# Performance work log

Measured on AMD Instinct MI355X. Metric: run time of the kernel, lower is better.

## Reference

```python
import jax, jax.numpy as jnp
import numpy as np

K = 12  # kNN neighbors (includes self, as in PyG knn(x, x, k))
EPS = 1e-5


def bn(h, g, b):
    # Training-mode BatchNorm over all axes except the last (feature) axis.
    ax = tuple(range(h.ndim - 1))
    m = h.mean(axis=ax, keepdims=True)
    v = h.var(axis=ax, keepdims=True)  # biased variance, as BN uses
    return g * (h - m) * jax.lax.rsqrt(v + EPS) + b


def edge_conv(x, W1, b1, g, be, W2, b2):
    # x: [B, N, C] -> [B, N, H]. Dynamic kNN graph in feature space per graph.
    d2 = jnp.sum(x * x, axis=-1)                                  # [B, N]
    dist = d2[:, :, None] + d2[:, None, :] - 2.0 * jnp.einsum('bic,bjc->bij', x, x)
    _, idx = jax.lax.top_k(-dist, K)                              # [B, N, K]
    xj = jnp.take_along_axis(x[:, None, :, :], idx[:, :, :, None], axis=2)  # [B,N,K,C]
    xi = jnp.broadcast_to(x[:, :, None, :], xj.shape)
    e = jnp.concatenate([xi, xj - xi], axis=-1)                   # [B,N,K,2C]
    h = jax.nn.relu(bn(jnp.einsum('bnkc,ch->bnkh', e, W1) + b1, g, be))
    h = jnp.einsum('bnkh,ho->bnko', h, W2) + b2
    return h.mean(axis=2)                                         # mean aggr over K


def setup_inputs() -> dict:
    key = jax.random.key(0)
    ks = jax.random.split(key, 8)
    B, N, C, H, Hf, O = 32, 1024, 3, 64, 32, 2
    s = 0.1
    return {
        'x': jax.random.normal(ks[0], (B, N, C), jnp.float32),
        'w0a': jax.random.normal(ks[1], (2 * C, H), jnp.float32) * s,
        'b0a': jnp.zeros((H,), jnp.float32),
        'g0': jnp.ones((H,), jnp.float32),
        'be0': jnp.zeros((H,), jnp.float32),
        'w0b': jax.random.normal(ks[2], (H, H), jnp.float32) * s,
        'b0b': jnp.zeros((H,), jnp.float32),
        'wa': jax.random.normal(ks[3], (3, 2 * H, H), jnp.float32) * s,
        'ba': jnp.zeros((3, H), jnp.float32),
        'ga': jnp.ones((3, H), jnp.float32),
        'bea': jnp.zeros((3, H), jnp.float32),
        'wb': jax.random.normal(ks[4], (3, H, H), jnp.float32) * s,
        'bb': jnp.zeros((3, H), jnp.float32),
        'wf1': jax.random.normal(ks[5], (H, Hf), jnp.float32) * s,
        'bf1': jnp.zeros((Hf,), jnp.float32),
        'gf': jnp.ones((Hf,), jnp.float32),
        'bef': jnp.zeros((Hf,), jnp.float32),
        'wf2': jax.random.normal(ks[6], (Hf, O), jnp.float32) * s,
        'bf2': jnp.zeros((O,), jnp.float32),
    }


def reference(x, w0a, b0a, g0, be0, w0b, b0b, wa, ba, ga, bea, wb, bb,
              wf1, bf1, gf, bef, wf2, bf2):
    # Layer 0: input channels = 3
    h = edge_conv(x, w0a, b0a, g0, be0, w0b, b0b)
    # Layers 1..3: input channels = hidden
    for i in range(3):
        h = edge_conv(h, wa[i], ba[i], ga[i], bea[i], wb[i], bb[i])
    pooled = h.mean(axis=1)  # global_mean_pool over nodes -> [B, H]
    z = jax.nn.relu(bn(pooled @ wf1 + bf1, gf, bef))
    return z @ wf2 + bf2     # [B, 2]
```

## Files before the change

kernel.cpp:

```cpp
#include <hip/hip_runtime.h>
#include <cstddef>

#define BATCH 32
#define NPTS  1024
#define K_NN  12
#define HID   64
#define BN_EPS 1e-5f

typedef short bf16x8 __attribute__((ext_vector_type(8)));
typedef float f32x4 __attribute__((ext_vector_type(4)));

__device__ __forceinline__ unsigned long long dkey(float dval, int j) {
  int di = __float_as_int(dval);
  unsigned m = (unsigned)(di >> 31) | 0x80000000u;
  unsigned u = (unsigned)di ^ m;
  return ((unsigned long long)u << 32) | (unsigned)j;
}

__device__ __forceinline__ void cas_u64(unsigned long long &a, unsigned long long &b) {
  unsigned long long x = a, y = b;
  bool c = y < x;
  a = c ? y : x;
  b = c ? x : y;
}

__device__ __forceinline__ void sort16_u64(unsigned long long (&k)[16]) {
  cas_u64(k[0],k[1]);  cas_u64(k[2],k[3]);  cas_u64(k[4],k[5]);  cas_u64(k[6],k[7]);
  cas_u64(k[8],k[9]);  cas_u64(k[10],k[11]); cas_u64(k[12],k[13]); cas_u64(k[14],k[15]);
  cas_u64(k[0],k[2]);  cas_u64(k[1],k[3]);  cas_u64(k[4],k[6]);  cas_u64(k[5],k[7]);
  cas_u64(k[8],k[10]); cas_u64(k[9],k[11]); cas_u64(k[12],k[14]); cas_u64(k[13],k[15]);
  cas_u64(k[1],k[2]);  cas_u64(k[5],k[6]);  cas_u64(k[9],k[10]); cas_u64(k[13],k[14]);
  cas_u64(k[0],k[4]);  cas_u64(k[1],k[5]);  cas_u64(k[2],k[6]);  cas_u64(k[3],k[7]);
  cas_u64(k[8],k[12]); cas_u64(k[9],k[13]); cas_u64(k[10],k[14]); cas_u64(k[11],k[15]);
  cas_u64(k[2],k[4]);  cas_u64(k[3],k[5]);  cas_u64(k[10],k[12]); cas_u64(k[11],k[13]);
  cas_u64(k[1],k[2]);  cas_u64(k[3],k[4]);  cas_u64(k[5],k[6]);
  cas_u64(k[9],k[10]); cas_u64(k[11],k[12]); cas_u64(k[13],k[14]);
  cas_u64(k[0],k[8]);  cas_u64(k[1],k[9]);  cas_u64(k[2],k[10]); cas_u64(k[3],k[11]);
  cas_u64(k[4],k[12]); cas_u64(k[5],k[13]); cas_u64(k[6],k[14]); cas_u64(k[7],k[15]);
  cas_u64(k[4],k[8]);  cas_u64(k[5],k[9]);  cas_u64(k[6],k[10]); cas_u64(k[7],k[11]);
  cas_u64(k[2],k[4]);  cas_u64(k[3],k[5]);  cas_u64(k[6],k[8]);  cas_u64(k[7],k[9]);
  cas_u64(k[10],k[12]); cas_u64(k[11],k[13]);
  cas_u64(k[1],k[2]);  cas_u64(k[3],k[4]);  cas_u64(k[5],k[6]);  cas_u64(k[7],k[8]);
  cas_u64(k[9],k[10]); cas_u64(k[11],k[12]); cas_u64(k[13],k[14]);
}

__device__ __forceinline__ void merge12_u64(unsigned long long (&L)[12],
                                            const unsigned long long* S) {
#pragma unroll
  for (int i = 0; i < 12; ++i) {
    unsigned long long s = S[11 - i];
    L[i] = L[i] < s ? L[i] : s;
  }
  cas_u64(L[0],L[8]);  cas_u64(L[1],L[9]);  cas_u64(L[2],L[10]); cas_u64(L[3],L[11]);
  cas_u64(L[4],L[8]);  cas_u64(L[5],L[9]);  cas_u64(L[6],L[10]); cas_u64(L[7],L[11]);
  cas_u64(L[0],L[2]);  cas_u64(L[1],L[3]);  cas_u64(L[4],L[6]);  cas_u64(L[5],L[7]);
  cas_u64(L[8],L[10]); cas_u64(L[9],L[11]);
  cas_u64(L[0],L[1]);  cas_u64(L[2],L[3]);  cas_u64(L[4],L[5]);  cas_u64(L[6],L[7]);
  cas_u64(L[8],L[9]);  cas_u64(L[10],L[11]);
}

__global__ __launch_bounds__(512, 2) void knn64_mfma_kernel(
    const unsigned short* __restrict__ xh, const unsigned short* __restrict__ xm,
    const unsigned short* __restrict__ xl, const float* __restrict__ d2,
    int* __restrict__ idx,
    const float* __restrict__ hxi, const float* __restrict__ hxj,
    float* __restrict__ partial) {
  const int b    = blockIdx.y;
  const int lane = threadIdx.x & 63;
  const int wv_u = __builtin_amdgcn_readfirstlane(threadIdx.x >> 6);
  const int i0   = blockIdx.x * 64;
  const size_t bbase = (size_t)b * NPTS;
  const float* d2b = d2 + bbase;

  constexpr int NE = 8 * K_NN;
  __shared__ __align__(16) char smem[60416];
  unsigned short* alds = (unsigned short*)smem;
  float* slab = (float*)(smem + 25600 + wv_u * 4352);
  unsigned long long* lk = (unsigned long long*)smem;
  int* jlds = (int*)(smem + 49664);
  float* red1 = (float*)smem;
  float* red2 = (float*)(smem + 2048);

  const int qr = lane >> 4;
  const int lr = lane & 15;

  for (int it = threadIdx.x; it < 1536; it += 512) {
    const int row = it / 24, rem = it % 24, pl = rem >> 3, seg = rem & 7;
    const unsigned short* src = (pl == 0) ? xh : ((pl == 1) ? xm : xl);
    *(bf16x8*)(alds + row * 200 + pl * 64 + seg * 8) =
        *(const bf16x8*)(src + (bbase + i0 + row) * HID + seg * 8);
  }
  __syncthreads();

  unsigned long long L[K_NN];
#pragma unroll
  for (int k = 0; k < K_NN; ++k) L[k] = ~0ULL;

  const int j0 = wv_u * 128;

  bf16x8 Bh0, Bh1, Bm0, Bm1, Bl0, Bl1;
  {
    const size_t brow = (bbase + j0 + lr) * HID;
    Bh0 = *(const bf16x8*)(xh + brow + 0  + qr * 8);
    Bh1 = *(const bf16x8*)(xh + brow + 32 + qr * 8);
    Bm0 = *(const bf16x8*)(xm + brow + 0  + qr * 8);
    Bm1 = *(const bf16x8*)(xm + brow + 32 + qr * 8);
    Bl0 = *(const bf16x8*)(xl + brow + 0  + qr * 8);
    Bl1 = *(const bf16x8*)(xl + brow + 32 + qr * 8);
  }

#pragma unroll 1
  for (int chunk = 0; chunk < 8; ++chunk) {
    const int jb = j0 + chunk * 16;
    const bf16x8 bh0 = Bh0, bh1 = Bh1, bm0 = Bm0, bm1 = Bm1, bl0 = Bl0, bl1 = Bl1;

    f32x4 acc[4];
#pragma unroll
    for (int isub = 0; isub < 4; ++isub) acc[isub] = f32x4{0.f, 0.f, 0.f, 0.f};

#pragma unroll
    for (int isub = 0; isub < 4; ++isub) {
      const int ar = (isub * 16 + lr) * 200;
      bf16x8 Ah0 = *(const bf16x8*)(alds + ar + 0   + qr * 8);
      bf16x8 Ah1 = *(const bf16x8*)(alds + ar + 32  + qr * 8);
      bf16x8 Am0 = *(const bf16x8*)(alds + ar + 64  + qr * 8);
      bf16x8 Am1 = *(const bf16x8*)(alds + ar + 96  + qr * 8);
      bf16x8 Al0 = *(const bf16x8*)(alds + ar + 128 + qr * 8);
      bf16x8 Al1 = *(const bf16x8*)(alds + ar + 160 + qr * 8);
      f32x4 a = acc[isub];
      a = __builtin_amdgcn_mfma_f32_16x16x32_bf16(Ah0, bh0, a, 0, 0, 0);
      a = __builtin_amdgcn_mfma_f32_16x16x32_bf16(Ah1, bh1, a, 0, 0, 0);
      a = __builtin_amdgcn_mfma_f32_16x16x32_bf16(Ah0, bm0, a, 0, 0, 0);
      a = __builtin_amdgcn_mfma_f32_16x16x32_bf16(Ah1, bm1, a, 0, 0, 0);
      a = __builtin_amdgcn_mfma_f32_16x16x32_bf16(Am0, bh0, a, 0, 0, 0);
      a = __builtin_amdgcn_mfma_f32_16x16x32_bf16(Am1, bh1, a, 0, 0, 0);
      a = __builtin_amdgcn_mfma_f32_16x16x32_bf16(Ah0, bl0, a, 0, 0, 0);
      a = __builtin_amdgcn_mfma_f32_16x16x32_bf16(Ah1, bl1, a, 0, 0, 0);
      a = __builtin_amdgcn_mfma_f32_16x16x32_bf16(Al0, bh0, a, 0, 0, 0);
      a = __builtin_amdgcn_mfma_f32_16x16x32_bf16(Al1, bh1, a, 0, 0, 0);
      a = __builtin_amdgcn_mfma_f32_16x16x32_bf16(Am0, bm0, a, 0, 0, 0);
      a = __builtin_amdgcn_mfma_f32_16x16x32_bf16(Am1, bm1, a, 0, 0, 0);
      acc[isub] = a;
    }

    if (chunk < 7) {
      const size_t nrow = (bbase + jb + 16 + lr) * HID;
      Bh0 = *(const bf16x8*)(xh + nrow + 0  + qr * 8);
      Bh1 = *(const bf16x8*)(xh + nrow + 32 + qr * 8);
      Bm0 = *(const bf16x8*)(xm + nrow + 0  + qr * 8);
      Bm1 = *(const bf16x8*)(xm + nrow + 32 + qr * 8);
      Bl0 = *(const bf16x8*)(xl + nrow + 0  + qr * 8);
      Bl1 = *(const bf16x8*)(xl + nrow + 32 + qr * 8);
    }

#pragma unroll
    for (int isub = 0; isub < 4; ++isub)
#pragma unroll
      for (int r = 0; r < 4; ++r)
        slab[(isub * 16 + qr * 4 + r) * 17 + lr] = acc[isub][r];

    unsigned long long S[16];
#pragma unroll
    for (int jj = 0; jj < 16; ++jj) {
      const int j = jb + jj;
      const float dot = slab[lane * 17 + jj];
      const float dval = fmaf(-2.f, dot, d2b[j]);
      S[jj] = dkey(dval, j);
    }
    sort16_u64(S);
    merge12_u64(L, S);
  }

  __syncthreads();
#pragma unroll
  for (int k = 0; k < K_NN; ++k)
    lk[lane * (NE + 1) + wv_u * K_NN + k] = L[k];
  __syncthreads();

  unsigned long long Lm[K_NN];
  if (wv_u < 2) {
    if (wv_u == 0) {
#pragma unroll
      for (int k = 0; k < K_NN; ++k) Lm[k] = L[k];
    } else {
#pragma unroll
      for (int k = 0; k < K_NN; ++k) Lm[k] = lk[lane * (NE + 1) + 4 * K_NN + k];
    }
#pragma unroll 1
    for (int w = 1; w < 4; ++w) {
      unsigned long long M[K_NN];
#pragma unroll
      for (int k = 0; k < K_NN; ++k)
        M[k] = lk[lane * (NE + 1) + (wv_u * 4 + w) * K_NN + k];
      merge12_u64(Lm, M);
    }
  }
  __syncthreads();
  if (wv_u == 1) {
#pragma unroll
    for (int k = 0; k < K_NN; ++k) lk[lane * (NE + 1) + 4 * K_NN + k] = Lm[k];
  }
  __syncthreads();
  if (wv_u == 0) {
    unsigned long long M[K_NN];
#pragma unroll
    for (int k = 0; k < K_NN; ++k) M[k] = lk[lane * (NE + 1) + 4 * K_NN + k];
    merge12_u64(Lm, M);
    int* op = idx + ((size_t)b * NPTS + i0 + lane) * K_NN;
#pragma unroll
    for (int k = 0; k < K_NN; ++k) {
      int jv = (int)(unsigned)(Lm[k] & 0xFFFFFFFFu);
      op[k] = jv;
      jlds[lane * K_NN + k] = jv;
    }
  }
  __syncthreads();

  {
    const float* hxib = hxi + (bbase + i0) * HID;
    const float* hxjb = hxj + bbase * HID;
    float s1 = 0.f, s2 = 0.f;
#pragma unroll 1
    for (int t = 0; t < 8; ++t) {
      const int nl = wv_u * 8 + t;
      const float hv = hxib[(size_t)nl * HID + lane];
      int jj[K_NN];
#pragma unroll
      for (int k = 0; k < K_NN; ++k) jj[k] = jlds[nl * K_NN + k];
      float v[K_NN];
#pragma unroll
      for (int k = 0; k < K_NN; ++k) v[k] = hxjb[(size_t)jj[k] * HID + lane];
#pragma unroll
      for (int k = 0; k < K_NN; ++k) {
        float h = hv + v[k];
        s1 += h;
        s2 = fmaf(h, h, s2);
      }
    }
    red1[wv_u * HID + lane] = s1;
    red2[wv_u * HID + lane] = s2;
  }
  __syncthreads();
  if (threadIdx.x < 128) {
    const int f = threadIdx.x & 63;
    const float* r = (threadIdx.x < 64) ? red1 : red2;
    float a = 0.f;
#pragma unroll
    for (int w = 0; w < 8; ++w) a += r[w * HID + f];
    partial[((size_t)b * 16 + blockIdx.x) * 128 + threadIdx.x] = a;
  }
}

__global__ __launch_bounds__(512, 2) void knn3_kernel(
    const float* __restrict__ x, const float* __restrict__ d2,
    int* __restrict__ idx,
    const float* __restrict__ hxi, const float* __restrict__ hxj,
    float* __restrict__ partial) {
  const int b    = blockIdx.y;
  const int lane = threadIdx.x & 63;
  const int wv_u = __builtin_amdgcn_readfirstlane(threadIdx.x >> 6);
  const int i0   = blockIdx.x * 64;
  const int i    = i0 + lane;
  const size_t bbase = (size_t)b * NPTS;
  const float* xb  = x  + bbase * 3;
  const float* d2b = d2 + bbase;

  constexpr int NE = 8 * K_NN;
  __shared__ __align__(16) char smem[53248];
  unsigned long long* lk = (unsigned long long*)smem;
  int* jlds = (int*)(smem + 49664);
  float* red1 = (float*)smem;
  float* red2 = (float*)(smem + 2048);

  float xi0 = xb[(size_t)i * 3 + 0];
  float xi1 = xb[(size_t)i * 3 + 1];
  float xi2v = xb[(size_t)i * 3 + 2];

  unsigned long long L[K_NN];
#pragma unroll
  for (int k = 0; k < K_NN; ++k) L[k] = ~0ULL;

  const int j0 = wv_u * 128;
#pragma unroll 1
  for (int ch = 0; ch < 8; ++ch) {
    unsigned long long S[16];
#pragma unroll
    for (int jj = 0; jj < 16; ++jj) {
      const int j = j0 + ch * 16 + jj;
      const float* xj = xb + (size_t)j * 3;
      const float d2j = d2b[j];
      float dot = fmaf(xi0, xj[0], 0.f);
      dot = fmaf(xi1, xj[1], dot);
      dot = fmaf(xi2v, xj[2], dot);
      S[jj] = dkey(fmaf(-2.f, dot, d2j), j);
    }
    sort16_u64(S);
    merge12_u64(L, S);
  }

#pragma unroll
  for (int k = 0; k < K_NN; ++k)
    lk[lane * (NE + 1) + wv_u * K_NN + k] = L[k];
  __syncthreads();

  unsigned long long Lm[K_NN];
  if (wv_u < 2) {
    if (wv_u == 0) {
#pragma unroll
      for (int k = 0; k < K_NN; ++k) Lm[k] = L[k];
    } else {
#pragma unroll
      for (int k = 0; k < K_NN; ++k) Lm[k] = lk[lane * (NE + 1) + 4 * K_NN + k];
    }
#pragma unroll 1
    for (int w = 1; w < 4; ++w) {
      unsigned long long M[K_NN];
#pragma unroll
      for (int k = 0; k < K_NN; ++k)
        M[k] = lk[lane * (NE + 1) + (wv_u * 4 + w) * K_NN + k];
      merge12_u64(Lm, M);
    }
  }
  __syncthreads();
  if (wv_u == 1) {
#pragma unroll
    for (int k = 0; k < K_NN; ++k) lk[lane * (NE + 1) + 4 * K_NN + k] = Lm[k];
  }
  __syncthreads();
  if (wv_u == 0) {
    unsigned long long M[K_NN];
#pragma unroll
    for (int k = 0; k < K_NN; ++k) M[k] = lk[lane * (NE + 1) + 4 * K_NN + k];
    merge12_u64(Lm, M);
    int* op = idx + ((size_t)b * NPTS + i0 + lane) * K_NN;
#pragma unroll
    for (int k = 0; k < K_NN; ++k) {
      int jv = (int)(unsigned)(Lm[k] & 0xFFFFFFFFu);
      op[k] = jv;
      jlds[lane * K_NN + k] = jv;
    }
  }
  __syncthreads();

  {
    const float* hxib = hxi + (bbase + i0) * HID;
    const float* hxjb2 = hxj + bbase * HID;
    float s1 = 0.f, s2 = 0.f;
#pragma unroll 1
    for (int t = 0; t < 8; ++t) {
      const int nl = wv_u * 8 + t;
      const float hv = hxib[(size_t)nl * HID + lane];
      int jj[K_NN];
#pragma unroll
      for (int k = 0; k < K_NN; ++k) jj[k] = jlds[nl * K_NN + k];
      float v[K_NN];
#pragma unroll
      for (int k = 0; k < K_NN; ++k) v[k] = hxjb2[(size_t)jj[k] * HID + lane];
#pragma unroll
      for (int k = 0; k < K_NN; ++k) {
        float h = hv + v[k];
        s1 += h;
        s2 = fmaf(h, h, s2);
      }
    }
    red1[wv_u * HID + lane] = s1;
    red2[wv_u * HID + lane] = s2;
  }
  __syncthreads();
  if (threadIdx.x < 128) {
    const int f = threadIdx.x & 63;
    const float* r = (threadIdx.x < 64) ? red1 : red2;
    float a = 0.f;
#pragma unroll
    for (int w = 0; w < 8; ++w) a += r[w * HID + f];
    partial[((size_t)b * 16 + blockIdx.x) * 128 + threadIdx.x] = a;
  }
}

__global__ __launch_bounds__(256) void rowgemm2_kernel(
    const float* __restrict__ X, const float* __restrict__ waL,
    const float* __restrict__ biasA,
    float* __restrict__ YA, float* __restrict__ YB) {
  __shared__ float wsa[HID * HID];
  __shared__ float wsb[HID * HID];
  for (int t = threadIdx.x; t < HID * HID; t += 256) {
    float wbv = waL[4096 + t];
    wsa[t] = waL[t] - wbv;
    wsb[t] = wbv;
  }
  __syncthreads();

  const int lane = threadIdx.x & 63;
  const int wv   = threadIdx.x >> 6;
  const int fq   = lane & 15;
  const int rg   = lane >> 4;
  const int r0   = blockIdx.x * 32 + wv * 8 + rg * 2;

  const float4* X4 = (const float4*)X;
  const float4* WA4 = (const float4*)wsa;
  const float4* WB4 = (const float4*)wsb;
  float aA0[4] = {0,0,0,0}, aA1[4] = {0,0,0,0};
  float aB0[4] = {0,0,0,0}, aB1[4] = {0,0,0,0};

#pragma unroll 2
  for (int cq = 0; cq < 16; ++cq) {
    float4 xa = X4[(size_t)r0 * 16 + cq];
    float4 xb_ = X4[(size_t)(r0 + 1) * 16 + cq];
    float ea[4] = {xa.x, xa.y, xa.z, xa.w};
    float eb[4] = {xb_.x, xb_.y, xb_.z, xb_.w};
#pragma unroll
    for (int d = 0; d < 4; ++d) {
      float4 wa4 = WA4[(cq * 4 + d) * 16 + fq];
      float4 wb4 = WB4[(cq * 4 + d) * 16 + fq];
      float wA[4] = {wa4.x, wa4.y, wa4.z, wa4.w};
      float wB[4] = {wb4.x, wb4.y, wb4.z, wb4.w};
#pragma unroll
      for (int k = 0; k < 4; ++k) {
        aA0[k] = fmaf(ea[d], wA[k], aA0[k]);
        aA1[k] = fmaf(eb[d], wA[k], aA1[k]);
        aB0[k] = fmaf(ea[d], wB[k], aB0[k]);
        aB1[k] = fmaf(eb[d], wB[k], aB1[k]);
      }
    }
  }
  float4 b4 = ((const float4*)biasA)[fq];
  float4 oA0{aA0[0] + b4.x, aA0[1] + b4.y, aA0[2] + b4.z, aA0[3] + b4.w};
  float4 oA1{aA1[0] + b4.x, aA1[1] + b4.y, aA1[2] + b4.z, aA1[3] + b4.w};
  float4 oB0{aB0[0], aB0[1], aB0[2], aB0[3]};
  float4 oB1{aB1[0], aB1[1], aB1[2], aB1[3]};
  ((float4*)YA)[(size_t)r0 * 16 + fq] = oA0;
  ((float4*)YA)[(size_t)(r0 + 1) * 16 + fq] = oA1;
  ((float4*)YB)[(size_t)r0 * 16 + fq] = oB0;
  ((float4*)YB)[(size_t)(r0 + 1) * 16 + fq] = oB1;
}

__global__ __launch_bounds__(256) void dual3_kernel(
    const float* __restrict__ x, const float* __restrict__ w0a,
    const float* __restrict__ b1,
    float* __restrict__ hxi, float* __restrict__ hxj,
    float* __restrict__ d2out) {
  __shared__ float Cs[3 * HID], Bs[3 * HID], bs[HID];
  for (int t = threadIdx.x; t < 3 * HID; t += 256) {
    float bv = w0a[192 + t];
    Cs[t] = w0a[t] - bv;
    Bs[t] = bv;
  }
  if (threadIdx.x < HID) bs[threadIdx.x] = b1[threadIdx.x];
  __syncthreads();

  const int lane = threadIdx.x & 63;
  const int wv   = __builtin_amdgcn_readfirstlane(threadIdx.x >> 6);
  const int node0 = blockIdx.x * 32;
#pragma unroll 1
  for (int it = 0; it < 8; ++it) {
    const int n = node0 + it * 4 + wv;
    const float* xr = x + (size_t)n * 3;
    float x0 = xr[0], x1 = xr[1], x2 = xr[2];
    float hi = bs[lane];
    hi = fmaf(x0, Cs[0 * HID + lane], hi);
    hi = fmaf(x1, Cs[1 * HID + lane], hi);
    hi = fmaf(x2, Cs[2 * HID + lane], hi);
    float hj = x0 * Bs[0 * HID + lane];
    hj = fmaf(x1, Bs[1 * HID + lane], hj);
    hj = fmaf(x2, Bs[2 * HID + lane], hj);
    hxi[(size_t)n * HID + lane] = hi;
    hxj[(size_t)n * HID + lane] = hj;
    if (lane == 0)
      d2out[n] = fmaf(x0, x0, fmaf(x1, x1, x2 * x2));
  }
}

__global__ __launch_bounds__(512) void bn_reduce_finalize_kernel(
    const float* __restrict__ g, const float* __restrict__ be,
    const float* __restrict__ partial, float* __restrict__ stats) {
  const int t   = threadIdx.x & 127;
  const int grp = threadIdx.x >> 7;
  float a0 = 0.f, a1 = 0.f, a2 = 0.f, a3 = 0.f;
  const int gb0 = grp * 128;
  for (int gb = gb0; gb < gb0 + 128; gb += 4) {
    a0 += partial[(size_t)(gb + 0) * 128 + t];
    a1 += partial[(size_t)(gb + 1) * 128 + t];
    a2 += partial[(size_t)(gb + 2) * 128 + t];
    a3 += partial[(size_t)(gb + 3) * 128 + t];
  }
  __shared__ float sm[4][128];
  sm[grp][t] = (a0 + a1) + (a2 + a3);
  __syncthreads();
  if (threadIdx.x < 128)
    sm[0][t] = (sm[0][t] + sm[1][t]) + (sm[2][t] + sm[3][t]);
  __syncthreads();
  if (threadIdx.x < HID) {
    const float inv_n = 1.f / (float)(BATCH * NPTS * K_NN);
    float m = sm[0][t] * inv_n;
    float v = sm[0][HID + t] * inv_n - m * m;
    float A = g[t] * rsqrtf(v + BN_EPS);
    stats[128 + t] = A;
    stats[192 + t] = be[t] - m * A;
  }
}

__global__ __launch_bounds__(256) void egapply_gemm_kernel(
    const int* __restrict__ idx, const float* __restrict__ hxi,
    const float* __restrict__ hxj, const float* __restrict__ stats,
    const float* __restrict__ W2, const float* __restrict__ b2,
    float* __restrict__ out, float* __restrict__ d2out,
    unsigned short* __restrict__ xsh, unsigned short* __restrict__ xsm,
    unsigned short* __restrict__ xsl, float* __restrict__ pooled) {
  __shared__ float w2s[HID * HID];
  __shared__ float red[32][HID];
  for (int t = threadIdx.x; t < HID * HID; t += 256) w2s[t] = W2[t];

  const int lane = threadIdx.x & 63;
  const int wv   = __builtin_amdgcn_readfirstlane(threadIdx.x >> 6);
  const int node0 = blockIdx.x * 32;
  const float A = stats[128 + lane], Bc = stats[192 + lane];

#pragma unroll 1
  for (int it = 0; it < 4; ++it) {
    const int n0 = node0 + it * 8 + wv;
    const int n1 = n0 + 4;
    const int bbase = (n0 >> 10) << 10;
    const int* ip0 = idx + (size_t)n0 * K_NN;
    const int* ip1 = idx + (size_t)n1 * K_NN;
    int j0[K_NN], j1[K_NN];
#pragma unroll
    for (int k = 0; k < K_NN; ++k) { j0[k] = ip0[k]; j1[k] = ip1[k]; }
    const float hv0 = hxi[(size_t)n0 * HID + lane];
    const float hv1 = hxi[(size_t)n1 * HID + lane];
    float v0[K_NN], v1[K_NN];
#pragma unroll
    for (int k = 0; k < K_NN; ++k) {
      v0[k] = hxj[(size_t)(bbase + j0[k]) * HID + lane];
      v1[k] = hxj[(size_t)(bbase + j1[k]) * HID + lane];
    }
    float a0 = 0.f, a1 = 0.f;
#pragma unroll
    for (int k = 0; k < K_NN; ++k) {
      a0 += fmaxf(fmaf(A, hv0 + v0[k], Bc), 0.f);
      a1 += fmaxf(fmaf(A, hv1 + v1[k], Bc), 0.f);
    }
    red[it * 8 + wv][lane] = a0;
    red[it * 8 + 4 + wv][lane] = a1;
  }
  __syncthreads();

  const float b2f = b2[lane];
  const float inv = 1.f / (float)K_NN;
  float psum = 0.f;
#pragma unroll 2
  for (int p = 0; p < 8; ++p) {
    int rr = p * 4 + wv;
    float acc0 = 0.f, acc1 = 0.f;
#pragma unroll 8
    for (int h = 0; h < HID; h += 2) {
      acc0 = fmaf(red[rr][h],     w2s[h * HID + lane],       acc0);
      acc1 = fmaf(red[rr][h + 1], w2s[(h + 1) * HID + lane], acc1);
    }
    float val = fmaf(acc0 + acc1, inv, b2f);
    const size_t o = (size_t)(node0 + rr) * HID + lane;
    out[o] = val;
    psum += val;

    unsigned u = __float_as_uint(val);
    unsigned short hh = (unsigned short)((u + 0x7FFFu + ((u >> 16) & 1u)) >> 16);
    float r1 = val - __uint_as_float((unsigned)hh << 16);
    unsigned ur = __float_as_uint(r1);
    unsigned short mm = (unsigned short)((ur + 0x7FFFu + ((ur >> 16) & 1u)) >> 16);
    float r2 = r1 - __uint_as_float((unsigned)mm << 16);
    unsigned ur2 = __float_as_uint(r2);
    unsigned short ll = (unsigned short)((ur2 + 0x7FFFu + ((ur2 >> 16) & 1u)) >> 16);
    xsh[o] = hh; xsm[o] = mm; xsl[o] = ll;

    float sq = val * val;
#pragma unroll
    for (int off = 1; off < 64; off <<= 1) sq += __shfl_xor(sq, off, 64);
    if (lane == 0) d2out[node0 + rr] = sq;
  }

  if (pooled != nullptr) {
    __syncthreads();
    red[wv][lane] = psum;
    __syncthreads();
    if (threadIdx.x < HID) {
      const int bb = node0 >> 10;
      float s = (red[0][lane] + red[1][lane]) + (red[2][lane] + red[3][lane]);
      atomicAdd(&pooled[bb * HID + lane], s * (1.f / (float)NPTS));
    }
  }
}

__global__ __launch_bounds__(256) void head_kernel(const float* __restrict__ pooled,
    const float* __restrict__ wf1, const float* __restrict__ bf1,
    const float* __restrict__ gf, const float* __restrict__ bef,
    const float* __restrict__ wf2, const float* __restrict__ bf2,
    float* __restrict__ out) {
  __shared__ float pl[BATCH * HID];
  __shared__ float t[BATCH * 32];
  __shared__ float Ab[32], Bb[32];
  for (int i = threadIdx.x; i < BATCH * HID; i += 256) pl[i] = pooled[i];
  __syncthreads();
  for (int i = threadIdx.x; i < BATCH * 32; i += 256) {
    int s = i >> 5, f1 = i & 31;
    float acc = bf1[f1];
    for (int h = 0; h < HID; ++h) acc = fmaf(pl[s * HID + h], wf1[h * 32 + f1], acc);
    t[i] = acc;
  }
  __syncthreads();
  if (threadIdx.x < 32) {
    int f1 = threadIdx.x;
    float m = 0.f;
    for (int s = 0; s < BATCH; ++s) m += t[s * 32 + f1];
    m *= (1.f / (float)BATCH);
    float v = 0.f;
    for (int s = 0; s < BATCH; ++s) { float d = t[s * 32 + f1] - m; v = fmaf(d, d, v); }
    v *= (1.f / (float)BATCH);
    float A = gf[f1] * rsqrtf(v + BN_EPS);
    Ab[f1] = A; Bb[f1] = bef[f1] - m * A;
  }
  __syncthreads();
  for (int i = threadIdx.x; i < BATCH * 32; i += 256) {
    int f1 = i & 31;
    t[i] = fmaxf(fmaf(Ab[f1], t[i], Bb[f1]), 0.f);
  }
  __syncthreads();
  if (threadIdx.x < BATCH * 2) {
    int s = threadIdx.x >> 1, o = threadIdx.x & 1;
    float acc = bf2[o];
    for (int f1 = 0; f1 < 32; ++f1) acc = fmaf(t[s * 32 + f1], wf2[f1 * 2 + o], acc);
    out[s * 2 + o] = acc;
  }
}

extern "C" void kernel_launch(void* const* d_in, const int* in_sizes, int n_in,
                              void* d_out, int out_size, void* d_ws, size_t ws_size,
                              hipStream_t stream) {
  const float* x   = (const float*)d_in[0];
  const float* w0a = (const float*)d_in[1];
  const float* b0a = (const float*)d_in[2];
  const float* g0  = (const float*)d_in[3];
  const float* be0 = (const float*)d_in[4];
  const float* w0b = (const float*)d_in[5];
  const float* b0b = (const float*)d_in[6];
  const float* wa  = (const float*)d_in[7];
  const float* ba  = (const float*)d_in[8];
  const float* ga  = (const float*)d_in[9];
  const float* bea = (const float*)d_in[10];
  const float* wb  = (const float*)d_in[11];
  const float* bb  = (const float*)d_in[12];
  const float* wf1 = (const float*)d_in[13];
  const float* bf1 = (const float*)d_in[14];
  const float* gf  = (const float*)d_in[15];
  const float* bef = (const float*)d_in[16];
  const float* wf2 = (const float*)d_in[17];
  const float* bf2 = (const float*)d_in[18];

  float* ws = (float*)d_ws;
  const size_t HN = (size_t)BATCH * NPTS * HID;
  const size_t ROWS = (size_t)BATCH * NPTS;
  float* bufA    = ws;
  float* bufB    = bufA + HN;
  float* hxi     = bufB + HN;
  float* hxjb    = hxi + HN;
  int*   idxb    = (int*)(hxjb + HN);
  float* d2buf   = (float*)(idxb + ROWS * K_NN);
  float* stats   = d2buf + ROWS;
  float* partial = stats + 256;
  float* pooled  = partial + 1024 * 128;
  unsigned short* xsh = (unsigned short*)(pooled + 2048);
  unsigned short* xsm = xsh + HN;
  unsigned short* xsl = xsm + HN;

  hipMemsetAsync(pooled, 0, BATCH * HID * sizeof(float), stream);

  dual3_kernel<<<1024, 256, 0, stream>>>(x, w0a, b0a, hxi, hxjb, d2buf);
  knn3_kernel<<<dim3(16, BATCH), 512, 0, stream>>>(x, d2buf, idxb, hxi, hxjb, partial);
  bn_reduce_finalize_kernel<<<1, 512, 0, stream>>>(g0, be0, partial, stats);
  egapply_gemm_kernel<<<1024, 256, 0, stream>>>(idxb, hxi, hxjb, stats, w0b, b0b,
                                                bufA, d2buf, xsh, xsm, xsl, nullptr);

  const float* cur = bufA;
  float* nxt = bufB;
  for (int i = 0; i < 3; ++i) {
    rowgemm2_kernel<<<(int)(ROWS / 32), 256, 0, stream>>>(cur, wa + (size_t)i * 8192,
                                                          ba + i * HID, hxi, hxjb);
    knn64_mfma_kernel<<<dim3(16, BATCH), 512, 0, stream>>>(xsh, xsm, xsl, d2buf, idxb,
                                                           hxi, hxjb, partial);
    bn_reduce_finalize_kernel<<<1, 512, 0, stream>>>(ga + i * HID, bea + i * HID, partial, stats);
    egapply_gemm_kernel<<<1024, 256, 0, stream>>>(idxb, hxi, hxjb, stats,
                                                  wb + (size_t)i * 4096, bb + i * HID,
                                                  nxt, d2buf, xsh, xsm, xsl,
                                                  (i == 2) ? pooled : nullptr);
    const float* t = cur; cur = nxt; nxt = (float*)t;
  }

  head_kernel<<<1, 256, 0, stream>>>(pooled, wf1, bf1, gf, bef, wf2, bf2, (float*)d_out);
}
```

Baseline: 496.2 us.

## Fuse BN stats finalize into egapply and shrink knn3 merge LDS

Removes the single-block bn_reduce_finalize kernel and has every egapply block redundantly reduce the 512x128 partial sums into BN scale and shift at startup. This saves four kernel launches and their serialization gaps, at the cost of each of 1024 blocks reading 256KB of partials, which should mostly hit in cache. Separately, the layer-0 knn3 kernel now merges per-wave top-12 lists as a tree (8→4→2→1) through a smaller LDS buffer. It also raises the launch bound to 4 blocks per CU to allow higher occupancy.

```diff
diff --git a/kernel.cpp b/kernel.cpp
--- a/kernel.cpp
+++ b/kernel.cpp
@@ -251,7 +251,7 @@
   }
 }
 
-__global__ __launch_bounds__(512, 2) void knn3_kernel(
+__global__ __launch_bounds__(512, 4) void knn3_kernel(
     const float* __restrict__ x, const float* __restrict__ d2,
     int* __restrict__ idx,
     const float* __restrict__ hxi, const float* __restrict__ hxj,
@@ -265,10 +265,9 @@
   const float* xb  = x  + bbase * 3;
   const float* d2b = d2 + bbase;
 
-  constexpr int NE = 8 * K_NN;
-  __shared__ __align__(16) char smem[53248];
-  unsigned long long* lk = (unsigned long long*)smem;
-  int* jlds = (int*)(smem + 49664);
+  __shared__ __align__(16) char smem[27648];
+  unsigned long long* buf = (unsigned long long*)smem;
+  int* jlds = (int*)(smem + 24576);
   float* red1 = (float*)smem;
   float* red2 = (float*)(smem + 2048);
 
@@ -298,44 +297,46 @@
     merge12_u64(L, S);
   }
 
-#pragma unroll
-  for (int k = 0; k < K_NN; ++k)
-    lk[lane * (NE + 1) + wv_u * K_NN + k] = L[k];
-  __syncthreads();
-
-  unsigned long long Lm[K_NN];
+  if (wv_u >= 4) {
+#pragma unroll
+    for (int k = 0; k < K_NN; ++k)
+      buf[((wv_u - 4) * 64 + lane) * K_NN + k] = L[k];
+  }
+  __syncthreads();
+  if (wv_u < 4) {
+    unsigned long long M[K_NN];
+#pragma unroll
+    for (int k = 0; k < K_NN; ++k) M[k] = buf[(wv_u * 64 + lane) * K_NN + k];
+    merge12_u64(L, M);
+  }
+  __syncthreads();
+  if (wv_u == 2 || wv_u == 3) {
+#pragma unroll
+    for (int k = 0; k < K_NN; ++k)
+      buf[((wv_u - 2) * 64 + lane) * K_NN + k] = L[k];
+  }
+  __syncthreads();
   if (wv_u < 2) {
-    if (wv_u == 0) {
-#pragma unroll
-      for (int k = 0; k < K_NN; ++k) Lm[k] = L[k];
-    } else {
-#pragma unroll
-      for (int k = 0; k < K_NN; ++k) Lm[k] = lk[lane * (NE + 1) + 4 * K_NN + k];
-    }
-#pragma unroll 1
-    for (int w = 1; w < 4; ++w) {
-      unsigned long long M[K_NN];
-#pragma unroll
-      for (int k = 0; k < K_NN; ++k)
-        M[k] = lk[lane * (NE + 1) + (wv_u * 4 + w) * K_NN + k];
-      merge12_u64(Lm, M);
-    }
+    unsigned long long M[K_NN];
+#pragma unroll
+    for (int k = 0; k < K_NN; ++k) M[k] = buf[(wv_u * 64 + lane) * K_NN + k];
+    merge12_u64(L, M);
   }
   __syncthreads();
   if (wv_u == 1) {
 #pragma unroll
-    for (int k = 0; k < K_NN; ++k) lk[lane * (NE + 1) + 4 * K_NN + k] = Lm[k];
+    for (int k = 0; k < K_NN; ++k) buf[lane * K_NN + k] = L[k];
   }
   __syncthreads();
   if (wv_u == 0) {
     unsigned long long M[K_NN];
 #pragma unroll
-    for (int k = 0; k < K_NN; ++k) M[k] = lk[lane * (NE + 1) + 4 * K_NN + k];
-    merge12_u64(Lm, M);
+    for (int k = 0; k < K_NN; ++k) M[k] = buf[lane * K_NN + k];
+    merge12_u64(L, M);
     int* op = idx + ((size_t)b * NPTS + i0 + lane) * K_NN;
 #pragma unroll
     for (int k = 0; k < K_NN; ++k) {
-      int jv = (int)(unsigned)(Lm[k] & 0xFFFFFFFFu);
+      int jv = (int)(unsigned)(L[k] & 0xFFFFFFFFu);
       op[k] = jv;
       jlds[lane * K_NN + k] = jv;
     }
@@ -470,50 +471,50 @@
   }
 }
 
-__global__ __launch_bounds__(512) void bn_reduce_finalize_kernel(
-    const float* __restrict__ g, const float* __restrict__ be,
-    const float* __restrict__ partial, float* __restrict__ stats) {
-  const int t   = threadIdx.x & 127;
-  const int grp = threadIdx.x >> 7;
-  float a0 = 0.f, a1 = 0.f, a2 = 0.f, a3 = 0.f;
-  const int gb0 = grp * 128;
-  for (int gb = gb0; gb < gb0 + 128; gb += 4) {
-    a0 += partial[(size_t)(gb + 0) * 128 + t];
-    a1 += partial[(size_t)(gb + 1) * 128 + t];
-    a2 += partial[(size_t)(gb + 2) * 128 + t];
-    a3 += partial[(size_t)(gb + 3) * 128 + t];
-  }
-  __shared__ float sm[4][128];
-  sm[grp][t] = (a0 + a1) + (a2 + a3);
-  __syncthreads();
-  if (threadIdx.x < 128)
-    sm[0][t] = (sm[0][t] + sm[1][t]) + (sm[2][t] + sm[3][t]);
-  __syncthreads();
-  if (threadIdx.x < HID) {
-    const float inv_n = 1.f / (float)(BATCH * NPTS * K_NN);
-    float m = sm[0][t] * inv_n;
-    float v = sm[0][HID + t] * inv_n - m * m;
-    float A = g[t] * rsqrtf(v + BN_EPS);
-    stats[128 + t] = A;
-    stats[192 + t] = be[t] - m * A;
-  }
-}
-
 __global__ __launch_bounds__(256) void egapply_gemm_kernel(
     const int* __restrict__ idx, const float* __restrict__ hxi,
-    const float* __restrict__ hxj, const float* __restrict__ stats,
+    const float* __restrict__ hxj, const float* __restrict__ partial,
+    const float* __restrict__ g, const float* __restrict__ be,
     const float* __restrict__ W2, const float* __restrict__ b2,
     float* __restrict__ out, float* __restrict__ d2out,
     unsigned short* __restrict__ xsh, unsigned short* __restrict__ xsm,
     unsigned short* __restrict__ xsl, float* __restrict__ pooled) {
   __shared__ float w2s[HID * HID];
   __shared__ float red[32][HID];
+  __shared__ float sAB[128];
   for (int t = threadIdx.x; t < HID * HID; t += 256) w2s[t] = W2[t];
 
   const int lane = threadIdx.x & 63;
   const int wv   = __builtin_amdgcn_readfirstlane(threadIdx.x >> 6);
   const int node0 = blockIdx.x * 32;
-  const float A = stats[128 + lane], Bc = stats[192 + lane];
+
+  {
+    const int t    = threadIdx.x & 127;
+    const int half = threadIdx.x >> 7;
+    float a0 = 0.f, a1 = 0.f, a2 = 0.f, a3 = 0.f;
+    const int gb0 = half * 256;
+    for (int gb = gb0; gb < gb0 + 256; gb += 4) {
+      a0 += partial[(size_t)(gb + 0) * 128 + t];
+      a1 += partial[(size_t)(gb + 1) * 128 + t];
+      a2 += partial[(size_t)(gb + 2) * 128 + t];
+      a3 += partial[(size_t)(gb + 3) * 128 + t];
+    }
+    float* sm = &red[0][0];
+    sm[half * 128 + t] = (a0 + a1) + (a2 + a3);
+    __syncthreads();
+    if (threadIdx.x < 128) sm[256 + t] = sm[t] + sm[128 + t];
+    __syncthreads();
+    if (threadIdx.x < HID) {
+      const float inv_n = 1.f / (float)(BATCH * NPTS * K_NN);
+      float m = sm[256 + threadIdx.x] * inv_n;
+      float v = sm[256 + HID + threadIdx.x] * inv_n - m * m;
+      float A = g[threadIdx.x] * rsqrtf(v + BN_EPS);
+      sAB[threadIdx.x] = A;
+      sAB[HID + threadIdx.x] = be[threadIdx.x] - m * A;
+    }
+    __syncthreads();
+  }
+  const float A = sAB[lane], Bc = sAB[HID + lane];
 
 #pragma unroll 1
   for (int it = 0; it < 4; ++it) {
@@ -674,9 +675,9 @@
 
   dual3_kernel<<<1024, 256, 0, stream>>>(x, w0a, b0a, hxi, hxjb, d2buf);
   knn3_kernel<<<dim3(16, BATCH), 512, 0, stream>>>(x, d2buf, idxb, hxi, hxjb, partial);
-  bn_reduce_finalize_kernel<<<1, 512, 0, stream>>>(g0, be0, partial, stats);
-  egapply_gemm_kernel<<<1024, 256, 0, stream>>>(idxb, hxi, hxjb, stats, w0b, b0b,
-                                                bufA, d2buf, xsh, xsm, xsl, nullptr);
+  egapply_gemm_kernel<<<1024, 256, 0, stream>>>(idxb, hxi, hxjb, partial, g0, be0,
+                                                w0b, b0b, bufA, d2buf,
+                                                xsh, xsm, xsl, nullptr);
 
   const float* cur = bufA;
   float* nxt = bufB;
@@ -685,8 +686,8 @@
                                                           ba + i * HID, hxi, hxjb);
     knn64_mfma_kernel<<<dim3(16, BATCH), 512, 0, stream>>>(xsh, xsm, xsl, d2buf, idxb,
                                                            hxi, hxjb, partial);
-    bn_reduce_finalize_kernel<<<1, 512, 0, stream>>>(ga + i * HID, bea + i * HID, partial, stats);
-    egapply_gemm_kernel<<<1024, 256, 0, stream>>>(idxb, hxi, hxjb, stats,
+    egapply_gemm_kernel<<<1024, 256, 0, stream>>>(idxb, hxi, hxjb, partial,
+                                                  ga + i * HID, bea + i * HID,
                                                   wb + (size_t)i * 4096, bb + i * HID,
                                                   nxt, d2buf, xsh, xsm, xsl,
                                                   (i == 2) ? pooled : nullptr);
```

After: 498.3 us. Within noise of the previous version (+0.4%).
